# Optimization experiments

Hardware: AMD Instinct MI355X
Metric: run time of the kernel (lower is better)

## Reference

```python
import jax, jax.numpy as jnp
import numpy as np

D_MODEL = 1024
NUM_HEADS = 16
HEAD_DIM = D_MODEL // NUM_HEADS
B, S = 4, 2048


def setup_inputs() -> dict:
    key = jax.random.key(0)
    ks = jax.random.split(key, 6)
    scale = 1.0 / np.sqrt(D_MODEL)
    return {
        "q": jax.random.normal(ks[0], (B, S, D_MODEL), dtype=jnp.float32),
        "k": jax.random.normal(ks[1], (B, S, D_MODEL), dtype=jnp.float32),
        "v": jax.random.normal(ks[2], (B, S, D_MODEL), dtype=jnp.float32),
        "Wq": jax.random.normal(ks[3], (D_MODEL, D_MODEL), dtype=jnp.float32) * scale,
        "Wk": jax.random.normal(ks[4], (D_MODEL, D_MODEL), dtype=jnp.float32) * scale,
        "Wv": jax.random.normal(ks[5], (D_MODEL, D_MODEL), dtype=jnp.float32) * scale,
    }


def reference(q, k, v, Wq, Wk, Wv):
    b, s, d = q.shape
    # nn.Linear(bias=False): x @ W.T
    qp = jnp.einsum('bsd,ed->bse', q, Wq)
    kp = jnp.einsum('bsd,ed->bse', k, Wk)
    vp = jnp.einsum('bsd,ed->bse', v, Wv)
    # split heads -> (B, H, S, Dh)
    qh = qp.reshape(b, s, NUM_HEADS, HEAD_DIM).transpose(0, 2, 1, 3)
    kh = kp.reshape(b, s, NUM_HEADS, HEAD_DIM).transpose(0, 2, 1, 3)
    vh = vp.reshape(b, s, NUM_HEADS, HEAD_DIM).transpose(0, 2, 1, 3)
    scores = jnp.einsum('bhqd,bhkd->bhqk', qh, kh) / jnp.sqrt(jnp.float32(HEAD_DIM))
    attn = jax.nn.softmax(scores, axis=-1)
    att = jnp.einsum('bhqk,bhkd->bhqd', attn, vh)
    # NOTE: faithful to the source, which does a raw .view (no head transpose back)
    return att.reshape(b, s, d)
```

## Files before the change

### kernel.cpp

```cpp
#include <hip/hip_runtime.h>
#include <hip/hip_bf16.h>
#include <stdint.h>

#define D_MODEL 1024
#define NHEAD   16
#define HDIM    64
#define BATCH   4
#define SEQ     2048
#define NTOK    (BATCH*SEQ)

typedef __bf16          b16x8 __attribute__((ext_vector_type(8)));
typedef unsigned short  u16x8 __attribute__((ext_vector_type(8)));
typedef unsigned short  u16x4 __attribute__((ext_vector_type(4)));
typedef float           f32x4 __attribute__((ext_vector_type(4)));

__device__ __forceinline__ unsigned short f2b(float f) {
  union { float f; uint32_t u; } c; c.f = f;
  return (unsigned short)((c.u + 0x7FFFu + ((c.u >> 16) & 1u)) >> 16);
}

__device__ __forceinline__ uint32_t cvtpk(float lo, float hi) {
  uint32_t r;
  asm("v_cvt_pk_bf16_f32 %0, %1, %2" : "=v"(r) : "v"(lo), "v"(hi));
  return r;
}

__device__ __forceinline__ b16x8 cv8(f32x4 a, f32x4 b) {
  b16x8 r;
#pragma unroll
  for (int i = 0; i < 4; i++) { r[i] = (__bf16)a[i]; r[i + 4] = (__bf16)b[i]; }
  return r;
}

__device__ __forceinline__ void glds16(const void* g, void* l) {
  __builtin_amdgcn_global_load_lds(
      (const __attribute__((address_space(1))) unsigned int*)g,
      (__attribute__((address_space(3))) unsigned int*)l, 16, 0, 0);
}

__global__ __launch_bounds__(256, 8)
void wpack_kernel(const float* __restrict__ Wq, const float* __restrict__ Wk,
                  const float* __restrict__ Wv, unsigned short* __restrict__ wsp) {
  int bid = blockIdx.x;
  int which = bid >> 8;
  int tn = (bid >> 5) & 7;
  int kt = bid & 31;
  const float* W = (which == 0) ? Wq : ((which == 1) ? Wk : Wv);
  int t = threadIdx.x;
  int r = t >> 1;
  int sw0 = (t & 1) * 2;
  char* dst = (char*)wsp + (size_t)bid * 8192 + t * 32;
  const float* src = W + (size_t)(tn * 128 + r) * D_MODEL + kt * 32;
#pragma unroll
  for (int i = 0; i < 2; i++) {
    int s = (sw0 + i) ^ ((r >> 1) & 3);
    f32x4 a = *(const f32x4*)(src + s * 8);
    f32x4 b = *(const f32x4*)(src + s * 8 + 4);
    u16x8 pk;
#pragma unroll
    for (int j = 0; j < 4; j++) { pk[j] = f2b(a[j]); pk[j + 4] = f2b(b[j]); }
    *(u16x8*)(dst + i * 16) = pk;
  }
}

__global__ __launch_bounds__(256, 3)
void proj_gemm_f32a(const float* __restrict__ q, const float* __restrict__ k,
                    const float* __restrict__ v, const unsigned short* __restrict__ wsp,
                    unsigned short* __restrict__ qp, unsigned short* __restrict__ kp,
                    unsigned short* __restrict__ vt) {
  __shared__ __align__(16) char lds[2][24576];

  int bid = blockIdx.x;
  int swz = (bid & 7) * 192 + (bid >> 3);
  int which = swz >> 9;
  int rr = swz & 511;
  int tm = rr >> 3, tn = rr & 7;

  const float* X = (which == 0) ? q : ((which == 1) ? k : v);
  const char* Bpack = (const char*)wsp + (size_t)((which * 8 + tn) * 32) * 8192;

  int tid  = threadIdx.x;
  int lane = tid & 63;
  int w    = tid >> 6;
  int g    = lane >> 4;
  int c    = lane & 15;
  int chi  = c & 7;
  int wr   = (w >> 1) * 64;
  int wc   = (w & 1) * 64;

  f32x4 acc[4][4];
#pragma unroll
  for (int m = 0; m < 4; m++)
#pragma unroll
    for (int n = 0; n < 4; n++) acc[m][n] = (f32x4){0.f, 0.f, 0.f, 0.f};

  int arowl = lane >> 3;
  int aswz  = ((lane & 7) ^ arowl) << 4;
  const char* Asrc = (const char*)(X + (size_t)(tm * 128 + w * 32 + arowl) * D_MODEL) + aswz;
  const char* Bsrc = Bpack + w * 2048 + lane * 16;

  int aoff0 = (wr + c) * 128 + ((2 * g    ^ chi) << 4);
  int aoff1 = (wr + c) * 128 + (((2*g+1) ^ chi) << 4);
  int rboff = 16384 + (wc + c) * 64 + ((g ^ ((c >> 1) & 3)) << 4);

#pragma unroll
  for (int i = 0; i < 4; i++)
    glds16(Asrc + (size_t)i * 8 * D_MODEL * 4, lds[0] + w * 4096 + i * 1024);
  glds16(Bsrc,        lds[0] + 16384 + w * 2048);
  glds16(Bsrc + 1024, lds[0] + 16384 + w * 2048 + 1024);

  for (int kt = 0; kt < 32; kt++) {
    __syncthreads();
    if (kt < 31) {
      char* nb = lds[(kt + 1) & 1];
#pragma unroll
      for (int i = 0; i < 4; i++)
        glds16(Asrc + (size_t)i * 8 * D_MODEL * 4 + (kt + 1) * 128, nb + w * 4096 + i * 1024);
      glds16(Bsrc + (size_t)(kt + 1) * 8192,        nb + 16384 + w * 2048);
      glds16(Bsrc + (size_t)(kt + 1) * 8192 + 1024, nb + 16384 + w * 2048 + 1024);
    }
    const char* buf = lds[kt & 1];
    b16x8 af[4];
    u16x8 bf[4];
#pragma unroll
    for (int m = 0; m < 4; m++) {
      f32x4 a0 = *(const f32x4*)(buf + aoff0 + m * 2048);
      f32x4 a1 = *(const f32x4*)(buf + aoff1 + m * 2048);
      af[m] = cv8(a0, a1);
    }
#pragma unroll
    for (int n = 0; n < 4; n++)
      bf[n] = *(const u16x8*)(buf + rboff + n * 1024);
#pragma unroll
    for (int m = 0; m < 4; m++)
#pragma unroll
      for (int n = 0; n < 4; n++)
        acc[m][n] = __builtin_amdgcn_mfma_f32_16x16x32_bf16(
            af[m], __builtin_bit_cast(b16x8, bf[n]), acc[m][n], 0, 0, 0);
  }

  int cbase = tn * 128 + wc;
  int rbase = tm * 128 + wr;
  if (which < 2) {
    unsigned short* OutP = (which == 0) ? qp : kp;
    float scale = (which == 0) ? 0.18033688f : 1.0f;
#pragma unroll
    for (int m = 0; m < 4; m++)
#pragma unroll
      for (int n = 0; n < 4; n++) {
        int e = cbase + n * 16 + c;
        int h = e >> 6, dh = e & 63;
#pragma unroll
        for (int j = 0; j < 4; j++) {
          int i = rbase + m * 16 + g * 4 + j;
          int b = i >> 11, s = i & 2047;
          OutP[(((size_t)(b * NHEAD + h)) * SEQ + s) * HDIM + dh] =
              f2b(acc[m][n][j] * scale);
        }
      }
  } else {
#pragma unroll
    for (int m = 0; m < 4; m++)
#pragma unroll
      for (int n = 0; n < 4; n++) {
        int e = cbase + n * 16 + c;
        int h = e >> 6, dh = e & 63;
        int i0 = rbase + m * 16 + g * 4;
        int b = i0 >> 11, s0 = i0 & 2047;
        u16x4 pk;
#pragma unroll
        for (int j = 0; j < 4; j++) pk[j] = f2b(acc[m][n][j]);
        *(u16x4*)&vt[(((size_t)(b * NHEAD + h)) * HDIM + dh) * SEQ + s0] = pk;
      }
  }
}

#define KVB 64
__global__ __launch_bounds__(256, 3)
void attn_kernel(const unsigned short* __restrict__ qp,
                 const unsigned short* __restrict__ kp,
                 const unsigned short* __restrict__ vt,
                 float* __restrict__ out) {
  __shared__ __align__(16) char lds[2][16384];

  int bid = blockIdx.x;
  int swz = (bid & 7) * 128 + (bid >> 3);
  int bh = swz >> 4;
  int qb = swz & 15;

  int tid  = threadIdx.x;
  int lane = tid & 63;
  int w    = tid >> 6;
  int g    = lane >> 4;
  int c    = lane & 15;
  int chi  = c & 7;

  const unsigned short* Kg = kp + (size_t)bh * SEQ * HDIM;
  const unsigned short* Vg = vt + (size_t)bh * HDIM * SEQ;

  int q0 = qb * 128 + w * 32;
  u16x8 qf[2][2];
#pragma unroll
  for (int qg = 0; qg < 2; qg++)
#pragma unroll
    for (int h = 0; h < 2; h++)
      qf[qg][h] = *(const u16x8*)&qp[((size_t)bh * SEQ + q0 + qg * 16 + c) * HDIM + h * 32 + g * 8];

  f32x4 o[4][2];
#pragma unroll
  for (int d = 0; d < 4; d++)
#pragma unroll
    for (int qg = 0; qg < 2; qg++) o[d][qg] = (f32x4){0.f, 0.f, 0.f, 0.f};
  f32x4 lacc[2];
  lacc[0] = (f32x4){0.f, 0.f, 0.f, 0.f};
  lacc[1] = (f32x4){0.f, 0.f, 0.f, 0.f};

  const u16x8 ones = {0x3F80, 0x3F80, 0x3F80, 0x3F80, 0x3F80, 0x3F80, 0x3F80, 0x3F80};

  int koffA = c * 128 + ((g * 16) ^ (chi << 4));
  int koffB = c * 128 + (((64 + g * 16)) ^ (chi << 4));
  int voff[2][2];
#pragma unroll
  for (int w2 = 0; w2 < 2; w2++) {
    int b0 = w2 * 64 + g * 8;
    voff[w2][0] = 8192 + c * 128 + ((((b0      >> 4) ^ chi) << 4) + (b0 & 15));
    voff[w2][1] = 8192 + c * 128 + (((((b0+32) >> 4) ^ chi) << 4) + (b0 & 15));
  }
  int arow = tid >> 3, aseg = tid & 7;
  int kwo = arow * 128 + ((aseg * 16) ^ ((arow & 7) << 4));
  int vwo = 8192 + kwo;

  char* cur = lds[0];
  char* nxt = lds[1];

  const unsigned short* KgP = Kg + (size_t)arow * HDIM + aseg * 8;
  const unsigned short* VgP = Vg + (size_t)arow * SEQ + aseg * 8;

  u16x8 kreg[2], vreg[2];
  kreg[0] = *(const u16x8*)(KgP);
  kreg[1] = *(const u16x8*)(KgP + 32 * HDIM);
  vreg[0] = *(const u16x8*)(VgP);
  vreg[1] = *(const u16x8*)(VgP + 32 * SEQ);
  *(u16x8*)(cur + kwo)        = kreg[0];
  *(u16x8*)(cur + kwo + 4096) = kreg[1];
  *(u16x8*)(cur + vwo)        = vreg[0];
  *(u16x8*)(cur + vwo + 4096) = vreg[1];
  __syncthreads();

  for (int t = 0; t < SEQ / KVB; t++) {
    if (t < SEQ / KVB - 1) {
      KgP += KVB * HDIM;
      VgP += KVB;
      kreg[0] = *(const u16x8*)(KgP);
      kreg[1] = *(const u16x8*)(KgP + 32 * HDIM);
      vreg[0] = *(const u16x8*)(VgP);
      vreg[1] = *(const u16x8*)(VgP + 32 * SEQ);
    }

    f32x4 sf[4][2];
    __builtin_amdgcn_s_setprio(1);
#pragma unroll
    for (int st = 0; st < 4; st++) {
      u16x8 kf0 = *(const u16x8*)(cur + koffA + st * 2048);
      u16x8 kf1 = *(const u16x8*)(cur + koffB + st * 2048);
#pragma unroll
      for (int qg = 0; qg < 2; qg++) {
        sf[st][qg] = __builtin_amdgcn_mfma_f32_16x16x32_bf16(
            __builtin_bit_cast(b16x8, kf0), __builtin_bit_cast(b16x8, qf[qg][0]),
            (f32x4){0.f, 0.f, 0.f, 0.f}, 0, 0, 0);
        sf[st][qg] = __builtin_amdgcn_mfma_f32_16x16x32_bf16(
            __builtin_bit_cast(b16x8, kf1), __builtin_bit_cast(b16x8, qf[qg][1]),
            sf[st][qg], 0, 0, 0);
      }
    }
    __builtin_amdgcn_s_setprio(0);

    union { uint32_t u[4]; u16x8 v; } pb[2][2];
#pragma unroll
    for (int qg = 0; qg < 2; qg++) {
      float p[4][4];
#pragma unroll
      for (int st = 0; st < 4; st++)
#pragma unroll
        for (int j = 0; j < 4; j++) p[st][j] = exp2f(sf[st][qg][j]);
#pragma unroll
      for (int w2 = 0; w2 < 2; w2++) {
        pb[w2][qg].u[0] = cvtpk(p[2*w2][0],   p[2*w2][1]);
        pb[w2][qg].u[1] = cvtpk(p[2*w2][2],   p[2*w2][3]);
        pb[w2][qg].u[2] = cvtpk(p[2*w2+1][0], p[2*w2+1][1]);
        pb[w2][qg].u[3] = cvtpk(p[2*w2+1][2], p[2*w2+1][3]);
      }
    }

    __builtin_amdgcn_s_setprio(1);
#pragma unroll
    for (int w2 = 0; w2 < 2; w2++) {
#pragma unroll
      for (int d = 0; d < 4; d++) {
        union { u16x4 h[2]; u16x8 v; } afu;
        afu.h[0] = *(const u16x4*)(cur + voff[w2][0] + d * 2048);
        afu.h[1] = *(const u16x4*)(cur + voff[w2][1] + d * 2048);
#pragma unroll
        for (int qg = 0; qg < 2; qg++)
          o[d][qg] = __builtin_amdgcn_mfma_f32_16x16x32_bf16(
              __builtin_bit_cast(b16x8, afu.v), __builtin_bit_cast(b16x8, pb[w2][qg].v),
              o[d][qg], 0, 0, 0);
      }
#pragma unroll
      for (int qg = 0; qg < 2; qg++)
        lacc[qg] = __builtin_amdgcn_mfma_f32_16x16x32_bf16(
            __builtin_bit_cast(b16x8, ones), __builtin_bit_cast(b16x8, pb[w2][qg].v),
            lacc[qg], 0, 0, 0);
    }
    __builtin_amdgcn_s_setprio(0);

    if (t < SEQ / KVB - 1) {
      *(u16x8*)(nxt + kwo)        = kreg[0];
      *(u16x8*)(nxt + kwo + 4096) = kreg[1];
      *(u16x8*)(nxt + vwo)        = vreg[0];
      *(u16x8*)(nxt + vwo + 4096) = vreg[1];
    }
    __syncthreads();
    char* tmp = cur; cur = nxt; nxt = tmp;
  }

#pragma unroll
  for (int qg = 0; qg < 2; qg++) {
    float inv = 1.f / lacc[qg][0];
    float* orow = out + ((size_t)bh * SEQ + q0 + qg * 16 + c) * HDIM;
#pragma unroll
    for (int d = 0; d < 4; d++) {
      f32x4 val;
#pragma unroll
      for (int j = 0; j < 4; j++) val[j] = o[d][qg][j] * inv;
      *(f32x4*)(orow + d * 16 + g * 4) = val;
    }
  }
}

extern "C" void kernel_launch(void* const* d_in, const int* in_sizes, int n_in,
                              void* d_out, int out_size, void* d_ws, size_t ws_size,
                              hipStream_t stream) {
  const float* q  = (const float*)d_in[0];
  const float* k  = (const float*)d_in[1];
  const float* v  = (const float*)d_in[2];
  const float* Wq = (const float*)d_in[3];
  const float* Wk = (const float*)d_in[4];
  const float* Wv = (const float*)d_in[5];

  const size_t projBytes = (size_t)NTOK * D_MODEL * 2;
  unsigned short* qp  = (unsigned short*)d_ws;
  unsigned short* kp  = (unsigned short*)((char*)d_ws + projBytes);
  unsigned short* vt  = (unsigned short*)((char*)d_ws + 2 * projBytes);
  unsigned short* wsp = (unsigned short*)((char*)d_ws + 3 * projBytes);
  float* out = (float*)d_out;

  hipLaunchKernelGGL(wpack_kernel, dim3(768), dim3(256), 0, stream,
                     Wq, Wk, Wv, wsp);
  hipLaunchKernelGGL(proj_gemm_f32a, dim3(1536), dim3(256), 0, stream,
                     q, k, v, wsp, qp, kp, vt);
  hipLaunchKernelGGL(attn_kernel, dim3(1024), dim3(256), 0, stream,
                     qp, kp, vt, out);
}
```

Before: 175.3 us.

## Stage K/V tiles with direct global-to-LDS loads and raise occupancy bound

Replaces the register-staged K/V double buffering in the attention kernel with direct global-to-LDS loads (glds16) into the alternate LDS buffer. The barrier moves to the top of each iteration, and a matching row/chunk XOR swizzle is applied on the global side. Skipping the staging registers frees VGPRs, so the launch bound goes from 3 to 4 waves per SIMD. The risk is that async LDS-DMA completion may not be covered by the barrier without an explicit vmcnt wait, and the higher occupancy bound may force register spills.

Result: no change. 173.0 us (-1.4%).

```diff
diff --git a/kernel.cpp b/kernel.cpp
--- a/kernel.cpp
+++ b/kernel.cpp
@@ -176,7 +176,7 @@
 }
 
 #define KVB 64
-__global__ __launch_bounds__(256, 3)
+__global__ __launch_bounds__(256, 4)
 void attn_kernel(const unsigned short* __restrict__ qp,
                  const unsigned short* __restrict__ kp,
                  const unsigned short* __restrict__ vt,
@@ -226,36 +226,29 @@
     voff[w2][0] = 8192 + c * 128 + ((((b0      >> 4) ^ chi) << 4) + (b0 & 15));
     voff[w2][1] = 8192 + c * 128 + (((((b0+32) >> 4) ^ chi) << 4) + (b0 & 15));
   }
-  int arow = tid >> 3, aseg = tid & 7;
-  int kwo = arow * 128 + ((aseg * 16) ^ ((arow & 7) << 4));
-  int vwo = 8192 + kwo;
-
-  char* cur = lds[0];
-  char* nxt = lds[1];
-
-  const unsigned short* KgP = Kg + (size_t)arow * HDIM + aseg * 8;
-  const unsigned short* VgP = Vg + (size_t)arow * SEQ + aseg * 8;
-
-  u16x8 kreg[2], vreg[2];
-  kreg[0] = *(const u16x8*)(KgP);
-  kreg[1] = *(const u16x8*)(KgP + 32 * HDIM);
-  vreg[0] = *(const u16x8*)(VgP);
-  vreg[1] = *(const u16x8*)(VgP + 32 * SEQ);
-  *(u16x8*)(cur + kwo)        = kreg[0];
-  *(u16x8*)(cur + kwo + 4096) = kreg[1];
-  *(u16x8*)(cur + vwo)        = vreg[0];
-  *(u16x8*)(cur + vwo + 4096) = vreg[1];
-  __syncthreads();
+
+  int srow   = lane >> 3;
+  int schunk = ((lane & 7) ^ srow) * 8;
+  const unsigned short* KgL = Kg + (size_t)(w * 16 + srow) * HDIM + schunk;
+  const unsigned short* VgL = Vg + (size_t)(w * 16 + srow) * SEQ + schunk;
+
+  glds16(KgL,           lds[0] + w * 2048);
+  glds16(KgL + 8 * HDIM, lds[0] + w * 2048 + 1024);
+  glds16(VgL,           lds[0] + 8192 + w * 2048);
+  glds16(VgL + 8 * SEQ,  lds[0] + 8192 + w * 2048 + 1024);
 
   for (int t = 0; t < SEQ / KVB; t++) {
+    __syncthreads();
     if (t < SEQ / KVB - 1) {
-      KgP += KVB * HDIM;
-      VgP += KVB;
-      kreg[0] = *(const u16x8*)(KgP);
-      kreg[1] = *(const u16x8*)(KgP + 32 * HDIM);
-      vreg[0] = *(const u16x8*)(VgP);
-      vreg[1] = *(const u16x8*)(VgP + 32 * SEQ);
-    }
+      KgL += KVB * HDIM;
+      VgL += KVB;
+      char* nb = lds[(t + 1) & 1];
+      glds16(KgL,            nb + w * 2048);
+      glds16(KgL + 8 * HDIM, nb + w * 2048 + 1024);
+      glds16(VgL,            nb + 8192 + w * 2048);
+      glds16(VgL + 8 * SEQ,  nb + 8192 + w * 2048 + 1024);
+    }
+    const char* cur = lds[t & 1];
 
     f32x4 sf[4][2];
     __builtin_amdgcn_s_setprio(1);
@@ -313,15 +306,6 @@
             lacc[qg], 0, 0, 0);
     }
     __builtin_amdgcn_s_setprio(0);
-
-    if (t < SEQ / KVB - 1) {
-      *(u16x8*)(nxt + kwo)        = kreg[0];
-      *(u16x8*)(nxt + kwo + 4096) = kreg[1];
-      *(u16x8*)(nxt + vwo)        = vreg[0];
-      *(u16x8*)(nxt + vwo + 4096) = vreg[1];
-    }
-    __syncthreads();
-    char* tmp = cur; cur = nxt; nxt = tmp;
   }
 
 #pragma unroll
```
